# Performance work log

Hardware: AMD Instinct MI355X
Metric: run time of the kernel (lower is better)

## Reference

```python
import jax, jax.numpy as jnp
import numpy as np

D_MODEL = 1024
N_HEAD = 16
D_K = D_MODEL // N_HEAD
B, T = 4, 2048


def setup_inputs() -> dict:
    key = jax.random.key(0)
    ks = jax.random.split(key, 12)
    s = 1.0 / np.sqrt(D_MODEL)
    inp = {
        "q": jax.random.normal(ks[0], (B, T, D_MODEL), jnp.float32),
        "k": jax.random.normal(ks[1], (B, T, D_MODEL), jnp.float32),
        "v": jax.random.normal(ks[2], (B, T, D_MODEL), jnp.float32),
        # causal mask: True = allowed
        "mask": jnp.tril(jnp.ones((T, T), bool))[None, None, :, :],
        "w_q": jax.random.uniform(ks[3], (D_MODEL, D_MODEL), jnp.float32, -s, s),
        "b_q": jax.random.uniform(ks[4], (D_MODEL,), jnp.float32, -s, s),
        "w_k": jax.random.uniform(ks[5], (D_MODEL, D_MODEL), jnp.float32, -s, s),
        "b_k": jax.random.uniform(ks[6], (D_MODEL,), jnp.float32, -s, s),
        "w_v": jax.random.uniform(ks[7], (D_MODEL, D_MODEL), jnp.float32, -s, s),
        "b_v": jax.random.uniform(ks[8], (D_MODEL,), jnp.float32, -s, s),
        "w_o": jax.random.uniform(ks[9], (D_MODEL, D_MODEL), jnp.float32, -s, s),
        "b_o": jax.random.uniform(ks[10], (D_MODEL,), jnp.float32, -s, s),
    }
    return inp


def reference(q, k, v, mask, w_q, b_q, w_k, b_k, w_v, b_v, w_o, b_o):
    b, tq, d = q.shape
    tk = k.shape[1]
    # projections (torch Linear: x @ W^T + b)
    qh = (q @ w_q.T + b_q).reshape(b, tq, N_HEAD, D_K).transpose(0, 2, 1, 3)
    kh = (k @ w_k.T + b_k).reshape(b, tk, N_HEAD, D_K).transpose(0, 2, 1, 3)
    vh = (v @ w_v.T + b_v).reshape(b, tk, N_HEAD, D_K).transpose(0, 2, 1, 3)
    # scores: (b, h, tq, tk)
    scores = jnp.einsum("bhqd,bhkd->bhqk", qh, kh) / jnp.sqrt(jnp.float32(D_K))
    scores = jnp.where(mask, scores, jnp.finfo(scores.dtype).min)
    attn = jax.nn.softmax(scores, axis=-1)
    out = jnp.einsum("bhqk,bhkd->bhqd", attn, vh)
    out = out.transpose(0, 2, 1, 3).reshape(b, tq, d)
    return out @ w_o.T + b_o
```

## Files before the change

### kernel.cpp

```cpp
#include <hip/hip_runtime.h>

typedef unsigned short u16;
typedef __attribute__((ext_vector_type(8))) short bf16x8;
typedef __attribute__((ext_vector_type(4))) float f32x4;

#define D_MODEL 1024
#define T_SEQ   2048
#define NB      4
#define NH      16
#define DKH     64

__device__ __forceinline__ u16 f2bf(float x) {
  union { float f; unsigned u; } v; v.f = x;
  unsigned r = v.u + 0x7fffu + ((v.u >> 16) & 1u);
  return (u16)(r >> 16);
}
__device__ __forceinline__ unsigned pack2(float a, float b) {
  return (unsigned)f2bf(a) | ((unsigned)f2bf(b) << 16);
}
__device__ __forceinline__ unsigned cvtpk2(float a, float b) {
  unsigned r;
  asm("v_cvt_pk_bf16_f32 %0, %1, %2" : "=v"(r) : "v"(a), "v"(b));
  return r;
}
__device__ __forceinline__ float fexp2(float x) {
#if __has_builtin(__builtin_amdgcn_exp2f)
  return __builtin_amdgcn_exp2f(x);
#else
  return __expf(x * 0.6931471805599453f);
#endif
}

__device__ __forceinline__ void gload16(const void* g, void* l) {
  __builtin_amdgcn_global_load_lds(
      (const __attribute__((address_space(1))) unsigned*)g,
      (__attribute__((address_space(3))) unsigned*)l, 16, 0, 0);
}

__global__ void cast_w4(const float* __restrict__ s0, const float* __restrict__ s1,
                        const float* __restrict__ s2, const float* __restrict__ s3,
                        u16* __restrict__ o0, u16* __restrict__ o1,
                        u16* __restrict__ o2, u16* __restrict__ o3) {
  const int which = blockIdx.y;
  const float* s = which == 0 ? s0 : which == 1 ? s1 : which == 2 ? s2 : s3;
  u16* o = which == 0 ? o0 : which == 1 ? o1 : which == 2 ? o2 : o3;
  int i = ((int)blockIdx.x * 256 + (int)threadIdx.x) * 4;
  float4 v = *(const float4*)(s + i);
  uint2 u; u.x = pack2(v.x, v.y); u.y = pack2(v.z, v.w);
  *(uint2*)(o + i) = u;
}

__global__ __launch_bounds__(256, 3) void gemm_qkv(
    const float* __restrict__ qin, const float* __restrict__ kin, const float* __restrict__ vin,
    const u16* __restrict__ wq, const u16* __restrict__ wk, const u16* __restrict__ wv,
    const float* __restrict__ bqp, const float* __restrict__ bkp, const float* __restrict__ bvp,
    u16* __restrict__ Xq, u16* __restrict__ Xk, u16* __restrict__ Xv) {
  const int z = blockIdx.z;
  const float* A = z == 0 ? qin : z == 1 ? kin : vin;
  const u16* W = z == 0 ? wq : z == 1 ? wk : wv;
  const float* bias = z == 0 ? bqp : z == 1 ? bkp : bvp;
  u16* C = z == 0 ? Xq : z == 1 ? Xk : Xv;
  const float osc = z == 0 ? 0.18033688011112042f : 1.0f;
  const int K = 1024, N = 1024;

  __shared__ __align__(16) char smem[49152];
  u16* As  = (u16*)smem;
  u16* Bs0 = (u16*)(smem + 16384);
  u16* Bs1 = (u16*)(smem + 32768);

  const int tid = threadIdx.x;
  const int w = tid >> 6, lane = tid & 63;
  const int wm = w & 1, wn = w >> 1;
  const int l15 = lane & 15, quad = lane >> 4;
  const int l8 = lane >> 3, l7 = lane & 7;
  const int m0 = blockIdx.x * 128, n0 = blockIdx.y * 128;
  const int sb = l7 ^ l8;

  const float* gA = A + (size_t)(m0 + w * 32 + l8) * K + sb * 8;
  const u16* gB = W + (size_t)(n0 + w * 32 + l8) * K + sb * 8;

  f32x4 zero4 = {0.f, 0.f, 0.f, 0.f};
  f32x4 acc[4][4];
#pragma unroll
  for (int i = 0; i < 4; ++i)
#pragma unroll
    for (int j = 0; j < 4; ++j) acc[i][j] = zero4;

#pragma unroll
  for (int j = 0; j < 4; ++j)
    gload16(gB + (size_t)(j * 8) * K, Bs0 + (w * 32 + j * 8) * 64);
  float4 a0[4], a1[4];
#pragma unroll
  for (int j = 0; j < 4; ++j) {
    const float* p = gA + (size_t)(j * 8) * K;
    a0[j] = *(const float4*)p;
    a1[j] = *(const float4*)(p + 4);
  }

  for (int kbi = 0; kbi < 16; ++kbi) {
    u16* Bc = (kbi & 1) ? Bs1 : Bs0;
    u16* Bn = (kbi & 1) ? Bs0 : Bs1;

    if (kbi) __syncthreads();

#pragma unroll
    for (int j = 0; j < 4; ++j) {
      uint4 wv4;
      wv4.x = cvtpk2(a0[j].x, a0[j].y); wv4.y = cvtpk2(a0[j].z, a0[j].w);
      wv4.z = cvtpk2(a1[j].x, a1[j].y); wv4.w = cvtpk2(a1[j].z, a1[j].w);
      *(uint4*)(As + (w * 32 + j * 8 + l8) * 64 + l7 * 8) = wv4;
    }
    __syncthreads();

    if (kbi < 15) {
      const int kb2 = (kbi + 1) * 64;
#pragma unroll
      for (int j = 0; j < 4; ++j)
        gload16(gB + kb2 + (size_t)(j * 8) * K, Bn + (w * 32 + j * 8) * 64);
#pragma unroll
      for (int j = 0; j < 4; ++j) {
        const float* p = gA + kb2 + (size_t)(j * 8) * K;
        a0[j] = *(const float4*)p;
        a1[j] = *(const float4*)(p + 4);
      }
      __builtin_amdgcn_sched_barrier(0);
    }

#pragma unroll
    for (int ks = 0; ks < 2; ++ks) {
      const int sw = ((ks * 4 + quad) ^ (l15 & 7)) * 8;
      bf16x8 af[4], bfr[4];
#pragma unroll
      for (int i = 0; i < 4; ++i)
        af[i] = *(const bf16x8*)(As + (wm * 64 + i * 16 + l15) * 64 + sw);
#pragma unroll
      for (int i = 0; i < 4; ++i)
        bfr[i] = *(const bf16x8*)(Bc + (wn * 64 + i * 16 + l15) * 64 + sw);
#pragma unroll
      for (int mi = 0; mi < 4; ++mi)
#pragma unroll
        for (int ni = 0; ni < 4; ++ni)
          acc[mi][ni] = __builtin_amdgcn_mfma_f32_16x16x32_bf16(af[mi], bfr[ni], acc[mi][ni], 0, 0, 0);
    }
  }

#pragma unroll
  for (int ni = 0; ni < 4; ++ni) {
    int col = n0 + wn * 64 + ni * 16 + l15;
    float bv = bias[col];
#pragma unroll
    for (int mi = 0; mi < 4; ++mi) {
      int row = m0 + wm * 64 + mi * 16 + quad * 4;
#pragma unroll
      for (int r = 0; r < 4; ++r)
        C[(size_t)(row + r) * N + col] = f2bf((acc[mi][ni][r] + bv) * osc);
    }
  }
}

__global__ __launch_bounds__(256) void gemm_nt_f32out(const u16* __restrict__ Ab,
                                                      const u16* __restrict__ W,
                                                      const float* __restrict__ bias,
                                                      float* __restrict__ Cp,
                                                      int M, int N, int K) {
  __shared__ __align__(16) u16 As[8192];
  __shared__ __align__(16) u16 Bs[8192];
  const int tid = threadIdx.x;
  const int w = tid >> 6, lane = tid & 63;
  const int wm = w & 1, wn = w >> 1;
  const int l15 = lane & 15, quad = lane >> 4;
  const int l8 = lane >> 3, l7 = lane & 7;
  const int m0 = blockIdx.x * 128, n0 = blockIdx.y * 128;
  const int sb = l7 ^ l8;

  const u16* gA = Ab + (size_t)(m0 + w * 32 + l8) * K + sb * 8;
  const u16* gB = W  + (size_t)(n0 + w * 32 + l8) * K + sb * 8;

  f32x4 zero4 = {0.f, 0.f, 0.f, 0.f};
  f32x4 acc[4][4];
#pragma unroll
  for (int i = 0; i < 4; ++i)
#pragma unroll
    for (int j = 0; j < 4; ++j) acc[i][j] = zero4;

  for (int kbi = 0; kbi < 16; ++kbi) {
    if (kbi) __syncthreads();
    const int kb = kbi * 64;
#pragma unroll
    for (int j = 0; j < 4; ++j) {
      gload16(gA + kb + (size_t)(j * 8) * K, As + (w * 32 + j * 8) * 64);
      gload16(gB + kb + (size_t)(j * 8) * K, Bs + (w * 32 + j * 8) * 64);
    }
    __syncthreads();

#pragma unroll
    for (int ks = 0; ks < 2; ++ks) {
      const int sw = ((ks * 4 + quad) ^ (l15 & 7)) * 8;
      bf16x8 af[4], bfr[4];
#pragma unroll
      for (int i = 0; i < 4; ++i)
        af[i] = *(const bf16x8*)(As + (wm * 64 + i * 16 + l15) * 64 + sw);
#pragma unroll
      for (int i = 0; i < 4; ++i)
        bfr[i] = *(const bf16x8*)(Bs + (wn * 64 + i * 16 + l15) * 64 + sw);
#pragma unroll
      for (int mi = 0; mi < 4; ++mi)
#pragma unroll
        for (int ni = 0; ni < 4; ++ni)
          acc[mi][ni] = __builtin_amdgcn_mfma_f32_16x16x32_bf16(af[mi], bfr[ni], acc[mi][ni], 0, 0, 0);
    }
  }

#pragma unroll
  for (int ni = 0; ni < 4; ++ni) {
    int col = n0 + wn * 64 + ni * 16 + l15;
    float bv = bias[col];
#pragma unroll
    for (int mi = 0; mi < 4; ++mi) {
      int row = m0 + wm * 64 + mi * 16 + quad * 4;
#pragma unroll
      for (int r = 0; r < 4; ++r)
        Cp[(size_t)(row + r) * N + col] = acc[mi][ni][r] + bv;
    }
  }
}

__global__ __launch_bounds__(512, 2) void attn_fwd(const u16* __restrict__ Xq,
                                                   const u16* __restrict__ Xk,
                                                   const u16* __restrict__ Xv,
                                                   u16* __restrict__ O) {
  __shared__ __align__(16) char smem[65536];

  const int xp = blockIdx.x;
  const int h = blockIdx.y, b = blockIdx.z;
  const int tid = threadIdx.x;
  const int w = tid >> 6, lane = tid & 63;
  const int half = w >> 2, wl = w & 3;
  const int l15 = lane & 15, quad = lane >> 4;
  const size_t base = (size_t)b * T_SEQ * D_MODEL;
  const int hd = h * DKH;

  u16* KtH = (u16*)(smem + half * 32768);
  u16* VtH = (u16*)(smem + half * 32768 + 16384);
  float* ML = (float*)(smem + 16384);
  float* MO = (float*)(smem + 32768);

  const int krow = lane >> 3;
  const int kcol = ((lane & 7) ^ krow) * 8;
  const u16* gK = Xk + base + (size_t)(wl * 16 + krow) * D_MODEL + hd + kcol;
  const int vkey = lane;
  const int skey = (vkey & 0x20) | ((vkey & 0xC) << 1) | ((vkey & 0x10) >> 2) | (vkey & 3);
  const int scb = skey >> 3, sci = skey & 7;
  const u16* gV = Xv + base + (size_t)vkey * D_MODEL + hd + wl * 16;

  bf16x8 bones;
#pragma unroll
  for (int i = 0; i < 8; ++i) bones[i] = (short)0x3F80;

  f32x4 zero4 = {0.f, 0.f, 0.f, 0.f};
  int tcnt = 0;

  {
    const u16* gk0 = gK + (size_t)(half * 64) * D_MODEL;
    gload16(gk0, KtH + (wl * 16) * 64);
    gload16(gk0 + (size_t)8 * D_MODEL, KtH + (wl * 16 + 8) * 64);
  }
  const u16* gv0 = gV + (size_t)(half * 64) * D_MODEL;
  uint4 va0 = *(const uint4*)gv0;
  uint4 va1 = *(const uint4*)(gv0 + 8);

  for (int ph = 0; ph < 2; ++ph) {
    const int qt = ph ? xp : 15 - xp;
    const int q0 = qt << 7;
    const int rowb0 = q0 + wl * 32;

    bf16x8 bq[2][2];
#pragma unroll
    for (int mi = 0; mi < 2; ++mi)
#pragma unroll
      for (int ks = 0; ks < 2; ++ks)
        bq[mi][ks] = *(const bf16x8*)(Xq + base + (size_t)(rowb0 + mi * 16 + l15) * D_MODEL
                                      + hd + ks * 32 + quad * 8);

    f32x4 o[4][2], ol[2];
#pragma unroll
    for (int di = 0; di < 4; ++di)
#pragma unroll
      for (int mi = 0; mi < 2; ++mi) o[di][mi] = zero4;
#pragma unroll
    for (int mi = 0; mi < 2; ++mi) ol[mi] = zero4;

    const int cnt = qt + 1;

    if (ph == 1 && half == 1) {
      const int fb = tcnt & 1;
      const u16* gk1 = gK + (size_t)64 * D_MODEL;
      gload16(gk1, KtH + fb * 4096 + (wl * 16) * 64);
      gload16(gk1 + (size_t)8 * D_MODEL, KtH + fb * 4096 + (wl * 16 + 8) * 64);
    }

    for (int i = 0; i < cnt; ++i, ++tcnt) {
      const int k0 = (half + 2 * i) * 64;
      const int buf = tcnt & 1;
      u16* ktb = KtH + buf * 4096;
      u16* vtb = VtH + buf * 4096;

      {
        union { uint4 u; u16 hh[8]; } u0, u1;
        u0.u = va0; u1.u = va1;
#pragma unroll
        for (int ii = 0; ii < 8; ++ii) {
          vtb[(wl * 16 + ii) * 64 + ((scb ^ ii) << 3) + sci] = u0.hh[ii];
          vtb[(wl * 16 + 8 + ii) * 64 + ((scb ^ ii) << 3) + sci] = u1.hh[ii];
        }
      }
      __syncthreads();

      const bool inph = (i + 1 < cnt);
      if (inph || ph == 0) {
        const int k0n = inph ? k0 + 128 : half * 64;
        if (inph || half == 0) {
          const u16* gk2 = gK + (size_t)k0n * D_MODEL;
          u16* ktn = KtH + (1 - buf) * 4096;
          gload16(gk2, ktn + (wl * 16) * 64);
          gload16(gk2 + (size_t)8 * D_MODEL, ktn + (wl * 16 + 8) * 64);
        }
        const u16* gv2 = gV + (size_t)k0n * D_MODEL;
        va0 = *(const uint4*)gv2;
        va1 = *(const uint4*)(gv2 + 8);
      }

      f32x4 st[4][2];
#pragma unroll
      for (int ni = 0; ni < 4; ++ni) {
        const u16* kr = ktb + (ni * 16 + l15) * 64;
        bf16x8 a0 = *(const bf16x8*)(kr + ((quad ^ (l15 & 7)) << 3));
        bf16x8 a1 = *(const bf16x8*)(kr + (((4 + quad) ^ (l15 & 7)) << 3));
#pragma unroll
        for (int mi = 0; mi < 2; ++mi) {
          f32x4 t = zero4;
          t = __builtin_amdgcn_mfma_f32_16x16x32_bf16(a0, bq[mi][0], t, 0, 0, 0);
          t = __builtin_amdgcn_mfma_f32_16x16x32_bf16(a1, bq[mi][1], t, 0, 0, 0);
          st[ni][mi] = t;
        }
      }

      bf16x8 bp[2][2];
#pragma unroll
      for (int mi = 0; mi < 2; ++mi) {
        const int qa = rowb0 + mi * 16 + l15;
        if (k0 + 63 > rowb0 + mi * 16) {
#pragma unroll
          for (int ni = 0; ni < 4; ++ni)
#pragma unroll
            for (int r = 0; r < 4; ++r)
              if (k0 + ni * 16 + quad * 4 + r > qa) st[ni][mi][r] = -1e30f;
        }
        float p[4][4];
#pragma unroll
        for (int ni = 0; ni < 4; ++ni)
#pragma unroll
          for (int r = 0; r < 4; ++r)
            p[ni][r] = fexp2(st[ni][mi][r]);
#pragma unroll
        for (int js = 0; js < 2; ++js) {
          union { bf16x8 v; unsigned d[4]; } ub;
          ub.d[0] = cvtpk2(p[2 * js][0], p[2 * js][1]);
          ub.d[1] = cvtpk2(p[2 * js][2], p[2 * js][3]);
          ub.d[2] = cvtpk2(p[2 * js + 1][0], p[2 * js + 1][1]);
          ub.d[3] = cvtpk2(p[2 * js + 1][2], p[2 * js + 1][3]);
          bp[mi][js] = ub.v;
        }
      }

#pragma unroll
      for (int js = 0; js < 2; ++js) {
        bf16x8 av[4];
#pragma unroll
        for (int di = 0; di < 4; ++di)
          av[di] = *(const bf16x8*)(vtb + (di * 16 + l15) * 64
                                    + (((js * 4 + quad) ^ (l15 & 7)) << 3));
#pragma unroll
        for (int di = 0; di < 4; ++di)
#pragma unroll
          for (int mi = 0; mi < 2; ++mi)
            o[di][mi] = __builtin_amdgcn_mfma_f32_16x16x32_bf16(av[di], bp[mi][js], o[di][mi], 0, 0, 0);
#pragma unroll
        for (int mi = 0; mi < 2; ++mi)
          ol[mi] = __builtin_amdgcn_mfma_f32_16x16x32_bf16(bones, bp[mi][js], ol[mi], 0, 0, 0);
      }
    }

    __syncthreads();
    if (half == 1) {
#pragma unroll
      for (int mi = 0; mi < 2; ++mi) {
        const int ql = wl * 32 + mi * 16 + l15;
        if (quad == 0) ML[ql] = ol[mi][0];
#pragma unroll
        for (int di = 0; di < 4; ++di)
#pragma unroll
          for (int r = 0; r < 4; ++r) {
            const int d = di * 16 + quad * 4 + r;
            MO[ql * 64 + (d ^ ((ql & 7) << 3))] = o[di][mi][r];
          }
      }
    }
    __syncthreads();
    if (half == 0) {
#pragma unroll
      for (int mi = 0; mi < 2; ++mi) {
        const int ql = wl * 32 + mi * 16 + l15;
        const float inv = 1.0f / (ol[mi][0] + ML[ql]);
        const size_t qa = q0 + ql;
#pragma unroll
        for (int di = 0; di < 4; ++di) {
          float t[4];
#pragma unroll
          for (int r = 0; r < 4; ++r) {
            const int d = di * 16 + quad * 4 + r;
            t[r] = (o[di][mi][r] + MO[ql * 64 + (d ^ ((ql & 7) << 3))]) * inv;
          }
          uint2 s2;
          s2.x = cvtpk2(t[0], t[1]);
          s2.y = cvtpk2(t[2], t[3]);
          *(uint2*)(O + base + qa * D_MODEL + hd + di * 16 + quad * 4) = s2;
        }
      }
    }
    __syncthreads();
  }
}

extern "C" void kernel_launch(void* const* d_in, const int* in_sizes, int n_in,
                              void* d_out, int out_size, void* d_ws, size_t ws_size,
                              hipStream_t stream) {
  const float* q   = (const float*)d_in[0];
  const float* k   = (const float*)d_in[1];
  const float* v   = (const float*)d_in[2];
  const float* w_q = (const float*)d_in[4];  const float* b_q = (const float*)d_in[5];
  const float* w_k = (const float*)d_in[6];  const float* b_k = (const float*)d_in[7];
  const float* w_v = (const float*)d_in[8];  const float* b_v = (const float*)d_in[9];
  const float* w_o = (const float*)d_in[10]; const float* b_o = (const float*)d_in[11];

  u16* ws = (u16*)d_ws;
  const size_t NTD = (size_t)NB * T_SEQ * D_MODEL;
  const size_t WSZ = (size_t)D_MODEL * D_MODEL;
  u16* wqb = ws;
  u16* wkb = wqb + WSZ;
  u16* wvb = wkb + WSZ;
  u16* wob = wvb + WSZ;
  u16* Xq  = wob + WSZ;
  u16* Xk  = Xq + NTD;
  u16* Xv  = Xk + NTD;
  u16* Ob  = Xv + NTD;

  cast_w4<<<dim3(WSZ / 1024, 4), 256, 0, stream>>>(w_q, w_k, w_v, w_o, wqb, wkb, wvb, wob);

  gemm_qkv<<<dim3(64, 8, 3), 256, 0, stream>>>(q, k, v, wqb, wkb, wvb,
                                               b_q, b_k, b_v, Xq, Xk, Xv);

  attn_fwd<<<dim3(8, NH, NB), 512, 0, stream>>>(Xq, Xk, Xv, Ob);

  gemm_nt_f32out<<<dim3(64, 8), 256, 0, stream>>>(Ob, wob, b_o, (float*)d_out,
                                                  8192, 1024, 1024);
}
```

Before: 316.5 us.

## Widen GEMM tiles to 128x256 with 512 threads and double-buffer output GEMM

Both projection GEMMs now use 512-thread blocks with a 128x256 output tile. Eight waves split the M and N dimensions, and the A tile loads are split across more waves. The output projection GEMM gains double-buffered LDS for A and B, with prefetch of the next k-block issued before compute. This increases reuse of each A tile and overlaps global loads with MFMA work. The cost is much larger LDS use per block (80-96KB), which lowers the number of resident blocks and halves the grid size.

```diff
diff --git a/kernel.cpp b/kernel.cpp
--- a/kernel.cpp
+++ b/kernel.cpp
@@ -50,7 +50,7 @@
   *(uint2*)(o + i) = u;
 }
 
-__global__ __launch_bounds__(256, 3) void gemm_qkv(
+__global__ __launch_bounds__(512, 4) void gemm_qkv(
     const float* __restrict__ qin, const float* __restrict__ kin, const float* __restrict__ vin,
     const u16* __restrict__ wq, const u16* __restrict__ wk, const u16* __restrict__ wv,
     const float* __restrict__ bqp, const float* __restrict__ bkp, const float* __restrict__ bvp,
@@ -63,20 +63,20 @@
   const float osc = z == 0 ? 0.18033688011112042f : 1.0f;
   const int K = 1024, N = 1024;
 
-  __shared__ __align__(16) char smem[49152];
+  __shared__ __align__(16) char smem[81920];
   u16* As  = (u16*)smem;
   u16* Bs0 = (u16*)(smem + 16384);
-  u16* Bs1 = (u16*)(smem + 32768);
+  u16* Bs1 = (u16*)(smem + 49152);
 
   const int tid = threadIdx.x;
   const int w = tid >> 6, lane = tid & 63;
   const int wm = w & 1, wn = w >> 1;
   const int l15 = lane & 15, quad = lane >> 4;
   const int l8 = lane >> 3, l7 = lane & 7;
-  const int m0 = blockIdx.x * 128, n0 = blockIdx.y * 128;
+  const int m0 = blockIdx.x * 128, n0 = blockIdx.y * 256;
   const int sb = l7 ^ l8;
 
-  const float* gA = A + (size_t)(m0 + w * 32 + l8) * K + sb * 8;
+  const float* gA = A + (size_t)(m0 + w * 16 + l8) * K + sb * 8;
   const u16* gB = W + (size_t)(n0 + w * 32 + l8) * K + sb * 8;
 
   f32x4 zero4 = {0.f, 0.f, 0.f, 0.f};
@@ -89,9 +89,9 @@
 #pragma unroll
   for (int j = 0; j < 4; ++j)
     gload16(gB + (size_t)(j * 8) * K, Bs0 + (w * 32 + j * 8) * 64);
-  float4 a0[4], a1[4];
-#pragma unroll
-  for (int j = 0; j < 4; ++j) {
+  float4 a0[2], a1[2];
+#pragma unroll
+  for (int j = 0; j < 2; ++j) {
     const float* p = gA + (size_t)(j * 8) * K;
     a0[j] = *(const float4*)p;
     a1[j] = *(const float4*)(p + 4);
@@ -104,11 +104,11 @@
     if (kbi) __syncthreads();
 
 #pragma unroll
-    for (int j = 0; j < 4; ++j) {
+    for (int j = 0; j < 2; ++j) {
       uint4 wv4;
       wv4.x = cvtpk2(a0[j].x, a0[j].y); wv4.y = cvtpk2(a0[j].z, a0[j].w);
       wv4.z = cvtpk2(a1[j].x, a1[j].y); wv4.w = cvtpk2(a1[j].z, a1[j].w);
-      *(uint4*)(As + (w * 32 + j * 8 + l8) * 64 + l7 * 8) = wv4;
+      *(uint4*)(As + (w * 16 + j * 8 + l8) * 64 + l7 * 8) = wv4;
     }
     __syncthreads();
 
@@ -118,7 +118,7 @@
       for (int j = 0; j < 4; ++j)
         gload16(gB + kb2 + (size_t)(j * 8) * K, Bn + (w * 32 + j * 8) * 64);
 #pragma unroll
-      for (int j = 0; j < 4; ++j) {
+      for (int j = 0; j < 2; ++j) {
         const float* p = gA + kb2 + (size_t)(j * 8) * K;
         a0[j] = *(const float4*)p;
         a1[j] = *(const float4*)(p + 4);
@@ -158,22 +158,26 @@
   }
 }
 
-__global__ __launch_bounds__(256) void gemm_nt_f32out(const u16* __restrict__ Ab,
-                                                      const u16* __restrict__ W,
-                                                      const float* __restrict__ bias,
-                                                      float* __restrict__ Cp,
-                                                      int M, int N, int K) {
-  __shared__ __align__(16) u16 As[8192];
-  __shared__ __align__(16) u16 Bs[8192];
+__global__ __launch_bounds__(512, 2) void gemm_nt_f32out(const u16* __restrict__ Ab,
+                                                         const u16* __restrict__ W,
+                                                         const float* __restrict__ bias,
+                                                         float* __restrict__ Cp,
+                                                         int M, int N, int K) {
+  __shared__ __align__(16) char smem[98304];
+  u16* As0 = (u16*)smem;
+  u16* As1 = (u16*)(smem + 16384);
+  u16* Bs0 = (u16*)(smem + 32768);
+  u16* Bs1 = (u16*)(smem + 65536);
+
   const int tid = threadIdx.x;
   const int w = tid >> 6, lane = tid & 63;
   const int wm = w & 1, wn = w >> 1;
   const int l15 = lane & 15, quad = lane >> 4;
   const int l8 = lane >> 3, l7 = lane & 7;
-  const int m0 = blockIdx.x * 128, n0 = blockIdx.y * 128;
+  const int m0 = blockIdx.x * 128, n0 = blockIdx.y * 256;
   const int sb = l7 ^ l8;
 
-  const u16* gA = Ab + (size_t)(m0 + w * 32 + l8) * K + sb * 8;
+  const u16* gA = Ab + (size_t)(m0 + w * 16 + l8) * K + sb * 8;
   const u16* gB = W  + (size_t)(n0 + w * 32 + l8) * K + sb * 8;
 
   f32x4 zero4 = {0.f, 0.f, 0.f, 0.f};
@@ -183,15 +187,31 @@
 #pragma unroll
     for (int j = 0; j < 4; ++j) acc[i][j] = zero4;
 
+#pragma unroll
+  for (int j = 0; j < 2; ++j)
+    gload16(gA + (size_t)(j * 8) * K, As0 + (w * 16 + j * 8) * 64);
+#pragma unroll
+  for (int j = 0; j < 4; ++j)
+    gload16(gB + (size_t)(j * 8) * K, Bs0 + (w * 32 + j * 8) * 64);
+
   for (int kbi = 0; kbi < 16; ++kbi) {
-    if (kbi) __syncthreads();
-    const int kb = kbi * 64;
-#pragma unroll
-    for (int j = 0; j < 4; ++j) {
-      gload16(gA + kb + (size_t)(j * 8) * K, As + (w * 32 + j * 8) * 64);
-      gload16(gB + kb + (size_t)(j * 8) * K, Bs + (w * 32 + j * 8) * 64);
-    }
+    u16* Ac = (kbi & 1) ? As1 : As0;
+    u16* An = (kbi & 1) ? As0 : As1;
+    u16* Bc = (kbi & 1) ? Bs1 : Bs0;
+    u16* Bn = (kbi & 1) ? Bs0 : Bs1;
+
     __syncthreads();
+
+    if (kbi < 15) {
+      const int kb2 = (kbi + 1) * 64;
+#pragma unroll
+      for (int j = 0; j < 2; ++j)
+        gload16(gA + kb2 + (size_t)(j * 8) * K, An + (w * 16 + j * 8) * 64);
+#pragma unroll
+      for (int j = 0; j < 4; ++j)
+        gload16(gB + kb2 + (size_t)(j * 8) * K, Bn + (w * 32 + j * 8) * 64);
+      __builtin_amdgcn_sched_barrier(0);
+    }
 
 #pragma unroll
     for (int ks = 0; ks < 2; ++ks) {
@@ -199,10 +219,10 @@
       bf16x8 af[4], bfr[4];
 #pragma unroll
       for (int i = 0; i < 4; ++i)
-        af[i] = *(const bf16x8*)(As + (wm * 64 + i * 16 + l15) * 64 + sw);
+        af[i] = *(const bf16x8*)(Ac + (wm * 64 + i * 16 + l15) * 64 + sw);
 #pragma unroll
       for (int i = 0; i < 4; ++i)
-        bfr[i] = *(const bf16x8*)(Bs + (wn * 64 + i * 16 + l15) * 64 + sw);
+        bfr[i] = *(const bf16x8*)(Bc + (wn * 64 + i * 16 + l15) * 64 + sw);
 #pragma unroll
       for (int mi = 0; mi < 4; ++mi)
 #pragma unroll
@@ -457,11 +477,11 @@
 
   cast_w4<<<dim3(WSZ / 1024, 4), 256, 0, stream>>>(w_q, w_k, w_v, w_o, wqb, wkb, wvb, wob);
 
-  gemm_qkv<<<dim3(64, 8, 3), 256, 0, stream>>>(q, k, v, wqb, wkb, wvb,
+  gemm_qkv<<<dim3(64, 4, 3), 512, 0, stream>>>(q, k, v, wqb, wkb, wvb,
                                                b_q, b_k, b_v, Xq, Xk, Xv);
 
   attn_fwd<<<dim3(8, NH, NB), 512, 0, stream>>>(Xq, Xk, Xv, Ob);
 
-  gemm_nt_f32out<<<dim3(64, 8), 256, 0, stream>>>(Ob, wob, b_o, (float*)d_out,
+  gemm_nt_f32out<<<dim3(64, 4), 512, 0, stream>>>(Ob, wob, b_o, (float*)d_out,
                                                   8192, 1024, 1024);
 }
```

New measurement: 325.8 us. +2.9%, slower.

## Double-buffer output-projection GEMM loads and raise MFMA priority in attention

Applied to the files above, without the earlier changes.

The f32-output GEMM now double-buffers the B tile in LDS and prefetches the next A tile into registers, so global loads for step k+1 overlap the MFMAs of step k. It also sets launch bounds to 3 blocks per CU with 48KB of LDS. Separately, the attention kernel wraps its QK and PV MFMA sections in s_setprio so waves in matrix phases get issue priority over waves doing softmax. Risks include higher register pressure from the prefetched A tile and an extra LDS store pass for A.

```diff
diff --git a/kernel.cpp b/kernel.cpp
--- a/kernel.cpp
+++ b/kernel.cpp
@@ -158,13 +158,16 @@
   }
 }
 
-__global__ __launch_bounds__(256) void gemm_nt_f32out(const u16* __restrict__ Ab,
-                                                      const u16* __restrict__ W,
-                                                      const float* __restrict__ bias,
-                                                      float* __restrict__ Cp,
-                                                      int M, int N, int K) {
-  __shared__ __align__(16) u16 As[8192];
-  __shared__ __align__(16) u16 Bs[8192];
+__global__ __launch_bounds__(256, 3) void gemm_nt_f32out(const u16* __restrict__ Ab,
+                                                         const u16* __restrict__ W,
+                                                         const float* __restrict__ bias,
+                                                         float* __restrict__ Cp,
+                                                         int M, int N, int K) {
+  __shared__ __align__(16) char smem[49152];
+  u16* As  = (u16*)smem;
+  u16* Bs0 = (u16*)(smem + 16384);
+  u16* Bs1 = (u16*)(smem + 32768);
+
   const int tid = threadIdx.x;
   const int w = tid >> 6, lane = tid & 63;
   const int wm = w & 1, wn = w >> 1;
@@ -183,15 +186,35 @@
 #pragma unroll
     for (int j = 0; j < 4; ++j) acc[i][j] = zero4;
 
+#pragma unroll
+  for (int j = 0; j < 4; ++j)
+    gload16(gB + (size_t)(j * 8) * K, Bs0 + (w * 32 + j * 8) * 64);
+  uint4 areg[4];
+#pragma unroll
+  for (int j = 0; j < 4; ++j)
+    areg[j] = *(const uint4*)(gA + (size_t)(j * 8) * K);
+
   for (int kbi = 0; kbi < 16; ++kbi) {
+    u16* Bc = (kbi & 1) ? Bs1 : Bs0;
+    u16* Bn = (kbi & 1) ? Bs0 : Bs1;
+
     if (kbi) __syncthreads();
-    const int kb = kbi * 64;
-#pragma unroll
-    for (int j = 0; j < 4; ++j) {
-      gload16(gA + kb + (size_t)(j * 8) * K, As + (w * 32 + j * 8) * 64);
-      gload16(gB + kb + (size_t)(j * 8) * K, Bs + (w * 32 + j * 8) * 64);
-    }
+
+#pragma unroll
+    for (int j = 0; j < 4; ++j)
+      *(uint4*)(As + (w * 32 + j * 8 + l8) * 64 + l7 * 8) = areg[j];
     __syncthreads();
+
+    if (kbi < 15) {
+      const int kb2 = (kbi + 1) * 64;
+#pragma unroll
+      for (int j = 0; j < 4; ++j)
+        gload16(gB + kb2 + (size_t)(j * 8) * K, Bn + (w * 32 + j * 8) * 64);
+#pragma unroll
+      for (int j = 0; j < 4; ++j)
+        areg[j] = *(const uint4*)(gA + kb2 + (size_t)(j * 8) * K);
+      __builtin_amdgcn_sched_barrier(0);
+    }
 
 #pragma unroll
     for (int ks = 0; ks < 2; ++ks) {
@@ -202,7 +225,7 @@
         af[i] = *(const bf16x8*)(As + (wm * 64 + i * 16 + l15) * 64 + sw);
 #pragma unroll
       for (int i = 0; i < 4; ++i)
-        bfr[i] = *(const bf16x8*)(Bs + (wn * 64 + i * 16 + l15) * 64 + sw);
+        bfr[i] = *(const bf16x8*)(Bc + (wn * 64 + i * 16 + l15) * 64 + sw);
 #pragma unroll
       for (int mi = 0; mi < 4; ++mi)
 #pragma unroll
@@ -331,6 +354,7 @@
       }
 
       f32x4 st[4][2];
+      __builtin_amdgcn_s_setprio(1);
 #pragma unroll
       for (int ni = 0; ni < 4; ++ni) {
         const u16* kr = ktb + (ni * 16 + l15) * 64;
@@ -344,6 +368,7 @@
           st[ni][mi] = t;
         }
       }
+      __builtin_amdgcn_s_setprio(0);
 
       bf16x8 bp[2][2];
 #pragma unroll
@@ -373,6 +398,7 @@
         }
       }
 
+      __builtin_amdgcn_s_setprio(1);
 #pragma unroll
       for (int js = 0; js < 2; ++js) {
         bf16x8 av[4];
@@ -389,6 +415,7 @@
         for (int mi = 0; mi < 2; ++mi)
           ol[mi] = __builtin_amdgcn_mfma_f32_16x16x32_bf16(bones, bp[mi][js], ol[mi], 0, 0, 0);
       }
+      __builtin_amdgcn_s_setprio(0);
     }
 
     __syncthreads();
```

Result: slower. 341.4 us (+7.9%).
